# Kernel tuning notes

Hardware: AMD Instinct MI355X
Metric: run time of the kernel (lower is better)

The kernel has to match this reference:

```python
import jax, jax.numpy as jnp
import numpy as np


def setup_inputs() -> dict:
    key = jax.random.key(0)
    ks = jax.random.split(key, 7)
    B, C, H, W = 8, 1024, 64, 64
    heads, head_dim, red = 8, 128, 8
    s = 1.0 / np.sqrt(head_dim)
    return {
        "x": jax.random.normal(ks[0], (B, C, H, W), jnp.float32),
        "Wq": jax.random.normal(ks[1], (heads, red, head_dim), jnp.float32) * s,
        "bq": jax.random.normal(ks[2], (heads, red), jnp.float32) * s,
        "Wk": jax.random.normal(ks[3], (heads, red, head_dim), jnp.float32) * s,
        "bk": jax.random.normal(ks[4], (heads, red), jnp.float32) * s,
        "Wv": jax.random.normal(ks[5], (heads, head_dim, head_dim), jnp.float32) * s,
        "bv": jax.random.normal(ks[6], (heads, head_dim), jnp.float32) * s,
    }


def reference(x, Wq, bq, Wk, bk, Wv, bv):
    B, C, H, W = x.shape
    heads, red, d = Wq.shape  # d = head_dim
    # (B, heads, head_dim, HW)
    xh = x.reshape(B, heads, d, H * W)
    # per-head spatial average pool: (B, heads, head_dim)
    avg = jnp.mean(xh, axis=-1)
    # torch Linear: y = x @ W.T + b, applied per head
    q = jnp.einsum("bhds,hrd->bhsr", xh, Wq) + bq[None, :, None, :]   # (B,H,S,r)
    k = jnp.einsum("bhd,hrd->bhr", avg, Wk) + bk[None]                 # (B,H,r)
    v = jnp.einsum("bhd,hed->bhe", avg, Wv) + bv[None]                 # (B,H,d)
    # single-key attention; softmax over the spatial dim (torch dim=1)
    scores = jnp.einsum("bhsr,bhr->bhs", q, k)                          # (B,H,S)
    attn = jax.nn.softmax(scores, axis=-1)
    out = jnp.einsum("bhs,bhe->bhes", attn, v)                          # (B,H,d,S)
    return out.reshape(B, C, H, W)
```

## Files before the change

kernel.cpp:

```cpp
#include <hip/hip_runtime.h>
#include <math.h>

#define SDIM 4096
#define DDIM 128
#define RED 8
#define BATCH 8
#define BH 64
#define CH 1024

typedef float vfloat4 __attribute__((ext_vector_type(4)));

#define WS_V   8192
#define WS_SC  16384

__inline__ __device__ float wave_reduce_sum(float v) {
#pragma unroll
    for (int o = 32; o > 0; o >>= 1) v += __shfl_down(v, o, 64);
    return v;
}
__inline__ __device__ float wave_reduce_max(float v) {
#pragma unroll
    for (int o = 32; o > 0; o >>= 1) v = fmaxf(v, __shfl_down(v, o, 64));
    return v;
}

__global__ __launch_bounds__(256) void k_avg(const float* __restrict__ x,
                                             float* __restrict__ ws) {
    const int row = blockIdx.x;
    const int t = threadIdx.x;
    const float4* xr = (const float4*)(x + (size_t)row * SDIM);
    float s = 0.f;
#pragma unroll
    for (int p = 0; p < 4; ++p) {
        float4 v = xr[t + 256 * p];
        s += v.x + v.y + v.z + v.w;
    }
    s = wave_reduce_sum(s);
    __shared__ float part[4];
    const int wave = t >> 6, lane = t & 63;
    if (lane == 0) part[wave] = s;
    __syncthreads();
    if (t == 0) {
        float tot = part[0] + part[1] + part[2] + part[3];
        ws[row] = tot * (1.0f / SDIM);
    }
}

__global__ __launch_bounds__(256) void k_scores(
        const float* __restrict__ x,
        const float* __restrict__ Wq, const float* __restrict__ bq,
        const float* __restrict__ Wk, const float* __restrict__ bk,
        float* __restrict__ ws) {
    const int blk = blockIdx.x;
    const int bh = blk >> 3, chunk = blk & 7;
    const int b = bh >> 3, h = bh & 7;
    const int t = threadIdx.x;

    __shared__ float avgs[DDIM];
    __shared__ float kk[RED];
    __shared__ float wqs[DDIM];
    __shared__ float cc;

    if (t < DDIM) avgs[t] = ws[b * CH + h * DDIM + t];
    __syncthreads();
    if (t < RED) {
        const float* wkr = Wk + (h * RED + t) * DDIM;
        float acc = 0.f;
#pragma unroll 8
        for (int d = 0; d < DDIM; ++d) acc += wkr[d] * avgs[d];
        kk[t] = acc + bk[h * RED + t];
    }
    __syncthreads();
    if (t < DDIM) {
        float acc = 0.f;
#pragma unroll
        for (int r = 0; r < RED; ++r) acc += Wq[(h * RED + r) * DDIM + t] * kk[r];
        wqs[t] = acc;
    }
    if (t == 0) {
        float acc = 0.f;
#pragma unroll
        for (int r = 0; r < RED; ++r) acc += bq[h * RED + r] * kk[r];
        cc = acc;
    }
    __syncthreads();

    const int s0 = chunk * 512 + t * 2;
    const float* xb = x + (size_t)(b * CH + h * DDIM) * SDIM + s0;
    float2 acc;
    const float c = cc;
    acc.x = c; acc.y = c;
#pragma unroll 16
    for (int d = 0; d < DDIM; ++d) {
        float2 xv = *(const float2*)(xb + (size_t)d * SDIM);
        const float w = wqs[d];
        acc.x += xv.x * w; acc.y += xv.y * w;
    }
    *(float2*)(ws + WS_SC + (size_t)bh * SDIM + s0) = acc;
}

__global__ __launch_bounds__(256) void k_softmax_v(
        const float* __restrict__ Wv, const float* __restrict__ bv,
        float* __restrict__ ws) {
    const int bh = blockIdx.x;
    const int b = bh >> 3, h = bh & 7;
    const int t = threadIdx.x;

    __shared__ float avgs[DDIM];
    if (t < DDIM) avgs[t] = ws[b * CH + h * DDIM + t];
    __syncthreads();
    if (t < DDIM) {
        const float* wvr = Wv + (h * DDIM + t) * DDIM;
        float acc = 0.f;
#pragma unroll 8
        for (int d = 0; d < DDIM; ++d) acc += wvr[d] * avgs[d];
        ws[WS_V + bh * DDIM + t] = acc + bv[h * DDIM + t];
    }

    float4* sc = (float4*)(ws + WS_SC + (size_t)bh * SDIM);
    float4 vals[4];
    float m = -1e30f;
#pragma unroll
    for (int p = 0; p < 4; ++p) {
        vals[p] = sc[t + 256 * p];
        m = fmaxf(m, fmaxf(fmaxf(vals[p].x, vals[p].y), fmaxf(vals[p].z, vals[p].w)));
    }
    m = wave_reduce_max(m);
    __shared__ float smax[4];
    __shared__ float ssum[4];
    const int wave = t >> 6, lane = t & 63;
    if (lane == 0) smax[wave] = m;
    __syncthreads();
    const float gm = fmaxf(fmaxf(smax[0], smax[1]), fmaxf(smax[2], smax[3]));
    float sum = 0.f;
#pragma unroll
    for (int p = 0; p < 4; ++p) {
        vals[p].x = expf(vals[p].x - gm);
        vals[p].y = expf(vals[p].y - gm);
        vals[p].z = expf(vals[p].z - gm);
        vals[p].w = expf(vals[p].w - gm);
        sum += vals[p].x + vals[p].y + vals[p].z + vals[p].w;
    }
    sum = wave_reduce_sum(sum);
    if (lane == 0) ssum[wave] = sum;
    __syncthreads();
    const float inv = 1.0f / (ssum[0] + ssum[1] + ssum[2] + ssum[3]);
#pragma unroll
    for (int p = 0; p < 4; ++p) {
        float4 o;
        o.x = vals[p].x * inv; o.y = vals[p].y * inv;
        o.z = vals[p].z * inv; o.w = vals[p].w * inv;
        sc[t + 256 * p] = o;
    }
}

__global__ __launch_bounds__(256) void k_out(const float* __restrict__ ws,
                                             float* __restrict__ out) {
    const vfloat4* attn = (const vfloat4*)(ws + WS_SC);
    const float* vv = ws + WS_V;
    const size_t total = (size_t)BATCH * CH * (SDIM / 4);
    const size_t stride = (size_t)gridDim.x * blockDim.x;
    for (size_t f = (size_t)blockIdx.x * blockDim.x + threadIdx.x; f < total; f += stride) {
        const int s4 = (int)(f & 1023);
        const int ce = (int)((f >> 10) & 1023);
        const int b = (int)(f >> 20);
        const int bh = (b << 3) | (ce >> 7);
        const int e = ce & 127;
        const vfloat4 a = attn[bh * 1024 + s4];
        const float vx = vv[bh * 128 + e];
        vfloat4 o = a * vx;
        __builtin_nontemporal_store(o, ((vfloat4*)out) + f);
    }
}

extern "C" void kernel_launch(void* const* d_in, const int* in_sizes, int n_in,
                              void* d_out, int out_size, void* d_ws, size_t ws_size,
                              hipStream_t stream) {
    const float* x  = (const float*)d_in[0];
    const float* Wq = (const float*)d_in[1];
    const float* bq = (const float*)d_in[2];
    const float* bk = (const float*)d_in[4];
    const float* Wk = (const float*)d_in[3];
    const float* Wv = (const float*)d_in[5];
    const float* bv = (const float*)d_in[6];
    float* out = (float*)d_out;
    float* ws  = (float*)d_ws;

    k_avg<<<8192, 256, 0, stream>>>(x, ws);
    k_scores<<<512, 256, 0, stream>>>(x, Wq, bq, Wk, bk, ws);
    k_softmax_v<<<BH, 256, 0, stream>>>(Wv, bv, ws);
    k_out<<<8192, 256, 0, stream>>>(ws, out);
}
```

Baseline: 270.5 us.

## Fuse pipeline into single-pass cooperative kernel with per-rank query projections

```diff
diff --git a/kernel.cpp b/kernel.cpp
--- a/kernel.cpp
+++ b/kernel.cpp
@@ -1,5 +1,8 @@
 #include <hip/hip_runtime.h>
+#include <hip/hip_cooperative_groups.h>
 #include <math.h>
+
+namespace cg = cooperative_groups;
 
 #define SDIM 4096
 #define DDIM 128
@@ -10,8 +13,11 @@
 
 typedef float vfloat4 __attribute__((ext_vector_type(4)));
 
-#define WS_V   8192
-#define WS_SC  16384
+#define WS_SMAX 65536
+#define WS_SSUM 66048
+#define WS_VV   66560
+#define WS_ATT  74752
+#define WS_QR   336896
 
 __inline__ __device__ float wave_reduce_sum(float v) {
 #pragma unroll
@@ -24,111 +30,255 @@
     return v;
 }
 
-__global__ __launch_bounds__(256) void k_avg(const float* __restrict__ x,
-                                             float* __restrict__ ws) {
-    const int row = blockIdx.x;
-    const int t = threadIdx.x;
-    const float4* xr = (const float4*)(x + (size_t)row * SDIM);
-    float s = 0.f;
-#pragma unroll
-    for (int p = 0; p < 4; ++p) {
-        float4 v = xr[t + 256 * p];
-        s += v.x + v.y + v.z + v.w;
-    }
-    s = wave_reduce_sum(s);
-    __shared__ float part[4];
-    const int wave = t >> 6, lane = t & 63;
-    if (lane == 0) part[wave] = s;
-    __syncthreads();
-    if (t == 0) {
-        float tot = part[0] + part[1] + part[2] + part[3];
-        ws[row] = tot * (1.0f / SDIM);
-    }
-}
-
-__global__ __launch_bounds__(256) void k_scores(
+__global__ __launch_bounds__(256, 2) void k_fused(
         const float* __restrict__ x,
         const float* __restrict__ Wq, const float* __restrict__ bq,
         const float* __restrict__ Wk, const float* __restrict__ bk,
+        const float* __restrict__ Wv, const float* __restrict__ bv,
+        float* __restrict__ ws, float* __restrict__ out) {
+    const int blk = blockIdx.x;
+    const int bh = blk >> 3, chunk = blk & 7;
+    const int h = bh & 7;
+    const int t = threadIdx.x;
+    const int wave = t >> 6, lane = t & 63;
+
+    __shared__ float wqt[DDIM * RED];
+    __shared__ float avgp[DDIM * 4];
+    __shared__ float avgs[DDIM];
+    __shared__ float kk[RED];
+    __shared__ float bqs[RED];
+    __shared__ float vvs[DDIM];
+    __shared__ float attn[512];
+    __shared__ float red4[4];
+    __shared__ float gM, gInv;
+
+    for (int i = t; i < DDIM * RED; i += 256) {
+        const int d = i >> 3, r = i & 7;
+        wqt[i] = Wq[(h * RED + r) * DDIM + d];
+    }
+    __syncthreads();
+
+    const int s0 = chunk * 512 + t * 2;
+    const float* xb = x + (size_t)bh * DDIM * SDIM + s0;
+    float2 acc[RED];
+#pragma unroll
+    for (int r = 0; r < RED; ++r) acc[r] = make_float2(0.f, 0.f);
+
+#pragma unroll 8
+    for (int d = 0; d < DDIM; ++d) {
+        const float2 xv = *(const float2*)(xb + (size_t)d * SDIM);
+        const float4 wa = *(const float4*)&wqt[d * 8];
+        const float4 wb = *(const float4*)&wqt[d * 8 + 4];
+        acc[0].x += xv.x * wa.x; acc[0].y += xv.y * wa.x;
+        acc[1].x += xv.x * wa.y; acc[1].y += xv.y * wa.y;
+        acc[2].x += xv.x * wa.z; acc[2].y += xv.y * wa.z;
+        acc[3].x += xv.x * wa.w; acc[3].y += xv.y * wa.w;
+        acc[4].x += xv.x * wb.x; acc[4].y += xv.y * wb.x;
+        acc[5].x += xv.x * wb.y; acc[5].y += xv.y * wb.y;
+        acc[6].x += xv.x * wb.z; acc[6].y += xv.y * wb.z;
+        acc[7].x += xv.x * wb.w; acc[7].y += xv.y * wb.w;
+        float px = wave_reduce_sum(xv.x + xv.y);
+        if (lane == 0) avgp[d * 4 + wave] = px;
+    }
+    __syncthreads();
+    if (t < DDIM)
+        ws[chunk * 8192 + bh * DDIM + t] =
+            avgp[t * 4] + avgp[t * 4 + 1] + avgp[t * 4 + 2] + avgp[t * 4 + 3];
+
+    cg::this_grid().sync();
+
+    if (t < DDIM) {
+        float a = 0.f;
+#pragma unroll
+        for (int c = 0; c < 8; ++c) a += ws[c * 8192 + bh * DDIM + t];
+        avgs[t] = a * (1.0f / SDIM);
+    }
+    __syncthreads();
+    if (t < RED) {
+        const float* wkr = Wk + (h * RED + t) * DDIM;
+        float a = 0.f;
+#pragma unroll 8
+        for (int d = 0; d < DDIM; ++d) a += wkr[d] * avgs[d];
+        kk[t] = a + bk[h * RED + t];
+        bqs[t] = bq[h * RED + t];
+    }
+    if (t < DDIM) {
+        const float* wvr = Wv + (h * DDIM + t) * DDIM;
+        float a = 0.f;
+#pragma unroll 8
+        for (int d = 0; d < DDIM; ++d) a += wvr[d] * avgs[d];
+        vvs[t] = a + bv[h * DDIM + t];
+    }
+    __syncthreads();
+
+    float c0 = 0.f;
+#pragma unroll
+    for (int r = 0; r < RED; ++r) c0 += bqs[r] * kk[r];
+    float2 sc = make_float2(c0, c0);
+#pragma unroll
+    for (int r = 0; r < RED; ++r) {
+        sc.x += acc[r].x * kk[r];
+        sc.y += acc[r].y * kk[r];
+    }
+
+    float m = wave_reduce_max(fmaxf(sc.x, sc.y));
+    if (lane == 0) red4[wave] = m;
+    __syncthreads();
+    const float bm = fmaxf(fmaxf(red4[0], red4[1]), fmaxf(red4[2], red4[3]));
+    float ps = expf(sc.x - bm) + expf(sc.y - bm);
+    ps = wave_reduce_sum(ps);
+    __syncthreads();
+    if (lane == 0) red4[wave] = ps;
+    __syncthreads();
+    if (t == 0) {
+        ws[WS_SMAX + blk] = bm;
+        ws[WS_SSUM + blk] = red4[0] + red4[1] + red4[2] + red4[3];
+    }
+
+    cg::this_grid().sync();
+
+    if (t == 0) {
+        float pm[8];
+        float M = -1e30f;
+#pragma unroll
+        for (int c = 0; c < 8; ++c) {
+            pm[c] = ws[WS_SMAX + bh * 8 + c];
+            M = fmaxf(M, pm[c]);
+        }
+        float S = 0.f;
+#pragma unroll
+        for (int c = 0; c < 8; ++c) S += ws[WS_SSUM + bh * 8 + c] * expf(pm[c] - M);
+        gM = M;
+        gInv = 1.0f / S;
+    }
+    __syncthreads();
+    float2 a2;
+    a2.x = expf(sc.x - gM) * gInv;
+    a2.y = expf(sc.y - gM) * gInv;
+    *(float2*)&attn[t * 2] = a2;
+    __syncthreads();
+
+    const vfloat4 a4 = ((const vfloat4*)attn)[t & 127];
+    float* ob = out + (size_t)bh * DDIM * SDIM + chunk * 512;
+    const int ehalf = t >> 7;
+#pragma unroll 8
+    for (int i = 0; i < 64; ++i) {
+        const int e = i * 2 + ehalf;
+        vfloat4 o = a4 * vvs[e];
+        __builtin_nontemporal_store(o, (vfloat4*)(ob + (size_t)e * SDIM) + (t & 127));
+    }
+}
+
+__global__ __launch_bounds__(256, 2) void k_pass1(
+        const float* __restrict__ x, const float* __restrict__ Wq,
         float* __restrict__ ws) {
     const int blk = blockIdx.x;
     const int bh = blk >> 3, chunk = blk & 7;
-    const int b = bh >> 3, h = bh & 7;
+    const int h = bh & 7;
     const int t = threadIdx.x;
-
-    __shared__ float avgs[DDIM];
-    __shared__ float kk[RED];
-    __shared__ float wqs[DDIM];
+    const int wave = t >> 6, lane = t & 63;
+
+    __shared__ float wqt[DDIM * RED];
+    __shared__ float avgp[DDIM * 4];
+
+    for (int i = t; i < DDIM * RED; i += 256) {
+        const int d = i >> 3, r = i & 7;
+        wqt[i] = Wq[(h * RED + r) * DDIM + d];
+    }
+    __syncthreads();
+
+    const int s0 = chunk * 512 + t * 2;
+    const float* xb = x + (size_t)bh * DDIM * SDIM + s0;
+    float2 acc[RED];
+#pragma unroll
+    for (int r = 0; r < RED; ++r) acc[r] = make_float2(0.f, 0.f);
+
+#pragma unroll 8
+    for (int d = 0; d < DDIM; ++d) {
+        const float2 xv = *(const float2*)(xb + (size_t)d * SDIM);
+        const float4 wa = *(const float4*)&wqt[d * 8];
+        const float4 wb = *(const float4*)&wqt[d * 8 + 4];
+        acc[0].x += xv.x * wa.x; acc[0].y += xv.y * wa.x;
+        acc[1].x += xv.x * wa.y; acc[1].y += xv.y * wa.y;
+        acc[2].x += xv.x * wa.z; acc[2].y += xv.y * wa.z;
+        acc[3].x += xv.x * wa.w; acc[3].y += xv.y * wa.w;
+        acc[4].x += xv.x * wb.x; acc[4].y += xv.y * wb.x;
+        acc[5].x += xv.x * wb.y; acc[5].y += xv.y * wb.y;
+        acc[6].x += xv.x * wb.z; acc[6].y += xv.y * wb.z;
+        acc[7].x += xv.x * wb.w; acc[7].y += xv.y * wb.w;
+        float px = wave_reduce_sum(xv.x + xv.y);
+        if (lane == 0) avgp[d * 4 + wave] = px;
+    }
+#pragma unroll
+    for (int r = 0; r < RED; ++r)
+        *(float2*)(ws + WS_QR + ((size_t)(bh * RED + r)) * SDIM + s0) = acc[r];
+    __syncthreads();
+    if (t < DDIM)
+        ws[chunk * 8192 + bh * DDIM + t] =
+            avgp[t * 4] + avgp[t * 4 + 1] + avgp[t * 4 + 2] + avgp[t * 4 + 3];
+}
+
+__global__ __launch_bounds__(256) void k_mid(
+        const float* __restrict__ bq, const float* __restrict__ Wk,
+        const float* __restrict__ bk, const float* __restrict__ Wv,
+        const float* __restrict__ bv, float* __restrict__ ws) {
+    const int bh = blockIdx.x;
+    const int h = bh & 7;
+    const int t = threadIdx.x;
+    const int wave = t >> 6, lane = t & 63;
+
+    __shared__ float avgs[DDIM], kk[RED], bqs[RED];
+    __shared__ float smax[4], ssum[4];
     __shared__ float cc;
 
-    if (t < DDIM) avgs[t] = ws[b * CH + h * DDIM + t];
+    if (t < DDIM) {
+        float a = 0.f;
+#pragma unroll
+        for (int c = 0; c < 8; ++c) a += ws[c * 8192 + bh * DDIM + t];
+        avgs[t] = a * (1.0f / SDIM);
+    }
     __syncthreads();
     if (t < RED) {
         const float* wkr = Wk + (h * RED + t) * DDIM;
-        float acc = 0.f;
-#pragma unroll 8
-        for (int d = 0; d < DDIM; ++d) acc += wkr[d] * avgs[d];
-        kk[t] = acc + bk[h * RED + t];
-    }
-    __syncthreads();
-    if (t < DDIM) {
-        float acc = 0.f;
-#pragma unroll
-        for (int r = 0; r < RED; ++r) acc += Wq[(h * RED + r) * DDIM + t] * kk[r];
-        wqs[t] = acc;
-    }
-    if (t == 0) {
-        float acc = 0.f;
-#pragma unroll
-        for (int r = 0; r < RED; ++r) acc += bq[h * RED + r] * kk[r];
-        cc = acc;
-    }
-    __syncthreads();
-
-    const int s0 = chunk * 512 + t * 2;
-    const float* xb = x + (size_t)(b * CH + h * DDIM) * SDIM + s0;
-    float2 acc;
-    const float c = cc;
-    acc.x = c; acc.y = c;
-#pragma unroll 16
-    for (int d = 0; d < DDIM; ++d) {
-        float2 xv = *(const float2*)(xb + (size_t)d * SDIM);
-        const float w = wqs[d];
-        acc.x += xv.x * w; acc.y += xv.y * w;
-    }
-    *(float2*)(ws + WS_SC + (size_t)bh * SDIM + s0) = acc;
-}
-
-__global__ __launch_bounds__(256) void k_softmax_v(
-        const float* __restrict__ Wv, const float* __restrict__ bv,
-        float* __restrict__ ws) {
-    const int bh = blockIdx.x;
-    const int b = bh >> 3, h = bh & 7;
-    const int t = threadIdx.x;
-
-    __shared__ float avgs[DDIM];
-    if (t < DDIM) avgs[t] = ws[b * CH + h * DDIM + t];
-    __syncthreads();
+        float a = 0.f;
+#pragma unroll 8
+        for (int d = 0; d < DDIM; ++d) a += wkr[d] * avgs[d];
+        kk[t] = a + bk[h * RED + t];
+        bqs[t] = bq[h * RED + t];
+    }
     if (t < DDIM) {
         const float* wvr = Wv + (h * DDIM + t) * DDIM;
-        float acc = 0.f;
-#pragma unroll 8
-        for (int d = 0; d < DDIM; ++d) acc += wvr[d] * avgs[d];
-        ws[WS_V + bh * DDIM + t] = acc + bv[h * DDIM + t];
-    }
-
-    float4* sc = (float4*)(ws + WS_SC + (size_t)bh * SDIM);
+        float a = 0.f;
+#pragma unroll 8
+        for (int d = 0; d < DDIM; ++d) a += wvr[d] * avgs[d];
+        ws[WS_VV + bh * DDIM + t] = a + bv[h * DDIM + t];
+    }
+    __syncthreads();
+    if (t == 0) {
+        float a = 0.f;
+#pragma unroll
+        for (int r = 0; r < RED; ++r) a += bqs[r] * kk[r];
+        cc = a;
+    }
+    __syncthreads();
+
+    const float4* qr4 = (const float4*)(ws + WS_QR + (size_t)bh * RED * SDIM);
     float4 vals[4];
     float m = -1e30f;
 #pragma unroll
     for (int p = 0; p < 4; ++p) {
-        vals[p] = sc[t + 256 * p];
-        m = fmaxf(m, fmaxf(fmaxf(vals[p].x, vals[p].y), fmaxf(vals[p].z, vals[p].w)));
+        float4 a;
+        a.x = cc; a.y = cc; a.z = cc; a.w = cc;
+#pragma unroll
+        for (int r = 0; r < RED; ++r) {
+            const float4 q = qr4[r * 1024 + t + 256 * p];
+            const float kr = kk[r];
+            a.x += q.x * kr; a.y += q.y * kr; a.z += q.z * kr; a.w += q.w * kr;
+        }
+        vals[p] = a;
+        m = fmaxf(m, fmaxf(fmaxf(a.x, a.y), fmaxf(a.z, a.w)));
     }
     m = wave_reduce_max(m);
-    __shared__ float smax[4];
-    __shared__ float ssum[4];
-    const int wave = t >> 6, lane = t & 63;
     if (lane == 0) smax[wave] = m;
     __syncthreads();
     const float gm = fmaxf(fmaxf(smax[0], smax[1]), fmaxf(smax[2], smax[3]));
@@ -145,19 +295,20 @@
     if (lane == 0) ssum[wave] = sum;
     __syncthreads();
     const float inv = 1.0f / (ssum[0] + ssum[1] + ssum[2] + ssum[3]);
+    float4* att4 = (float4*)(ws + WS_ATT + (size_t)bh * SDIM);
 #pragma unroll
     for (int p = 0; p < 4; ++p) {
         float4 o;
         o.x = vals[p].x * inv; o.y = vals[p].y * inv;
         o.z = vals[p].z * inv; o.w = vals[p].w * inv;
-        sc[t + 256 * p] = o;
-    }
-}
-
-__global__ __launch_bounds__(256) void k_out(const float* __restrict__ ws,
-                                             float* __restrict__ out) {
-    const vfloat4* attn = (const vfloat4*)(ws + WS_SC);
-    const float* vv = ws + WS_V;
+        att4[t + 256 * p] = o;
+    }
+}
+
+__global__ __launch_bounds__(256) void k_bcast(const float* __restrict__ ws,
+                                               float* __restrict__ out) {
+    const vfloat4* attn = (const vfloat4*)(ws + WS_ATT);
+    const float* vv = ws + WS_VV;
     const size_t total = (size_t)BATCH * CH * (SDIM / 4);
     const size_t stride = (size_t)gridDim.x * blockDim.x;
     for (size_t f = (size_t)blockIdx.x * blockDim.x + threadIdx.x; f < total; f += stride) {
@@ -179,15 +330,20 @@
     const float* x  = (const float*)d_in[0];
     const float* Wq = (const float*)d_in[1];
     const float* bq = (const float*)d_in[2];
+    const float* Wk = (const float*)d_in[3];
     const float* bk = (const float*)d_in[4];
-    const float* Wk = (const float*)d_in[3];
     const float* Wv = (const float*)d_in[5];
     const float* bv = (const float*)d_in[6];
     float* out = (float*)d_out;
     float* ws  = (float*)d_ws;
 
-    k_avg<<<8192, 256, 0, stream>>>(x, ws);
-    k_scores<<<512, 256, 0, stream>>>(x, Wq, bq, Wk, bk, ws);
-    k_softmax_v<<<BH, 256, 0, stream>>>(Wv, bv, ws);
-    k_out<<<8192, 256, 0, stream>>>(ws, out);
-}
+    void* args[] = {(void*)&x, (void*)&Wq, (void*)&bq, (void*)&Wk, (void*)&bk,
+                    (void*)&Wv, (void*)&bv, (void*)&ws, (void*)&out};
+    hipError_t err = hipLaunchCooperativeKernel((const void*)k_fused, dim3(512),
+                                                dim3(256), args, 0, stream);
+    if (err != hipSuccess) {
+        k_pass1<<<512, 256, 0, stream>>>(x, Wq, ws);
+        k_mid<<<BH, 256, 0, stream>>>(bq, Wk, bk, Wv, bv, ws);
+        k_bcast<<<8192, 256, 0, stream>>>(ws, out);
+    }
+}
```

After: 428.1 us. +58.3%, slower.

## Fuse average pooling with per-rank query projection in one pass over x

Applied to the files above, without the earlier changes.

```diff
diff --git a/kernel.cpp b/kernel.cpp
--- a/kernel.cpp
+++ b/kernel.cpp
@@ -10,8 +10,11 @@
 
 typedef float vfloat4 __attribute__((ext_vector_type(4)));
 
-#define WS_V   8192
-#define WS_SC  16384
+#define WS_AVG  0
+#define WS_VV   32768
+#define WS_ATT  40960
+#define WS_QRP  303104
+#define QRP_DG  2097152
 
 __inline__ __device__ float wave_reduce_sum(float v) {
 #pragma unroll
@@ -24,111 +27,138 @@
     return v;
 }
 
-__global__ __launch_bounds__(256) void k_avg(const float* __restrict__ x,
-                                             float* __restrict__ ws) {
-    const int row = blockIdx.x;
-    const int t = threadIdx.x;
-    const float4* xr = (const float4*)(x + (size_t)row * SDIM);
-    float s = 0.f;
-#pragma unroll
-    for (int p = 0; p < 4; ++p) {
-        float4 v = xr[t + 256 * p];
-        s += v.x + v.y + v.z + v.w;
-    }
-    s = wave_reduce_sum(s);
-    __shared__ float part[4];
-    const int wave = t >> 6, lane = t & 63;
-    if (lane == 0) part[wave] = s;
-    __syncthreads();
-    if (t == 0) {
-        float tot = part[0] + part[1] + part[2] + part[3];
-        ws[row] = tot * (1.0f / SDIM);
-    }
-}
-
-__global__ __launch_bounds__(256) void k_scores(
-        const float* __restrict__ x,
-        const float* __restrict__ Wq, const float* __restrict__ bq,
-        const float* __restrict__ Wk, const float* __restrict__ bk,
+__global__ __launch_bounds__(256, 4) void k_qr(
+        const float* __restrict__ x, const float* __restrict__ Wq,
         float* __restrict__ ws) {
     const int blk = blockIdx.x;
-    const int bh = blk >> 3, chunk = blk & 7;
-    const int b = bh >> 3, h = bh & 7;
+    const int dg = blk & 3, chunk = (blk >> 2) & 3, bh = blk >> 4;
+    const int h = bh & 7;
     const int t = threadIdx.x;
-
-    __shared__ float avgs[DDIM];
-    __shared__ float kk[RED];
-    __shared__ float wqs[DDIM];
+    const int wave = t >> 6, lane = t & 63;
+    const int r8 = lane >> 3, seg = lane & 7;
+
+    __shared__ float wqt[32 * 8];
+    __shared__ float sxy[4][8][65];
+    __shared__ float fpart[4][4][8][9];
+
+    wqt[t] = Wq[(h * RED + (t & 7)) * DDIM + dg * 32 + (t >> 3)];
+    __syncthreads();
+
+    const int s0 = chunk * 1024 + t * 4;
+    const float* xb = x + (size_t)(bh * DDIM + dg * 32) * SDIM + s0;
+    vfloat4 accq[RED];
+#pragma unroll
+    for (int r = 0; r < RED; ++r) accq[r] = (vfloat4)0.f;
+
+#pragma unroll
+    for (int g = 0; g < 4; ++g) {
+#pragma unroll
+        for (int j = 0; j < 8; ++j) {
+            const int dl = g * 8 + j;
+            const vfloat4 xv = *(const vfloat4*)(xb + (size_t)dl * SDIM);
+            const float4 wa = *(const float4*)&wqt[dl * 8];
+            const float4 wb = *(const float4*)&wqt[dl * 8 + 4];
+            accq[0] += xv * wa.x;
+            accq[1] += xv * wa.y;
+            accq[2] += xv * wa.z;
+            accq[3] += xv * wa.w;
+            accq[4] += xv * wb.x;
+            accq[5] += xv * wb.y;
+            accq[6] += xv * wb.z;
+            accq[7] += xv * wb.w;
+            sxy[wave][j][lane] = xv[0] + xv[1] + xv[2] + xv[3];
+        }
+        float ps = 0.f;
+#pragma unroll
+        for (int j = 0; j < 8; ++j) ps += sxy[wave][r8][seg * 8 + j];
+        fpart[wave][g][r8][seg] = ps;
+    }
+
+    float* qb = ws + WS_QRP + (size_t)dg * QRP_DG + (size_t)(bh * RED) * SDIM + s0;
+#pragma unroll
+    for (int r = 0; r < RED; ++r)
+        *(vfloat4*)(qb + (size_t)r * SDIM) = accq[r];
+
+    __syncthreads();
+    if (t < 32) {
+        const int g = t >> 3, rr = t & 7;
+        float a = 0.f;
+#pragma unroll
+        for (int w = 0; w < 4; ++w)
+#pragma unroll
+            for (int s2 = 0; s2 < 8; ++s2)
+                a += fpart[w][g][rr][s2];
+        ws[WS_AVG + chunk * 8192 + bh * DDIM + dg * 32 + t] = a;
+    }
+}
+
+__global__ __launch_bounds__(256) void k_head(
+        const float* __restrict__ bq, const float* __restrict__ Wk,
+        const float* __restrict__ bk, const float* __restrict__ Wv,
+        const float* __restrict__ bv, float* __restrict__ ws) {
+    const int bh = blockIdx.x;
+    const int h = bh & 7;
+    const int t = threadIdx.x;
+    const int wave = t >> 6, lane = t & 63;
+
+    __shared__ float avgs[DDIM], kk[RED], bqs[RED];
+    __shared__ float smax[4], ssum[4];
     __shared__ float cc;
 
-    if (t < DDIM) avgs[t] = ws[b * CH + h * DDIM + t];
+    if (t < DDIM) {
+        float a = 0.f;
+#pragma unroll
+        for (int c = 0; c < 4; ++c) a += ws[WS_AVG + c * 8192 + bh * DDIM + t];
+        avgs[t] = a * (1.0f / SDIM);
+    }
     __syncthreads();
     if (t < RED) {
         const float* wkr = Wk + (h * RED + t) * DDIM;
-        float acc = 0.f;
+        float a = 0.f;
 #pragma unroll 8
-        for (int d = 0; d < DDIM; ++d) acc += wkr[d] * avgs[d];
-        kk[t] = acc + bk[h * RED + t];
-    }
-    __syncthreads();
-    if (t < DDIM) {
-        float acc = 0.f;
-#pragma unroll
-        for (int r = 0; r < RED; ++r) acc += Wq[(h * RED + r) * DDIM + t] * kk[r];
-        wqs[t] = acc;
-    }
-    if (t == 0) {
-        float acc = 0.f;
-#pragma unroll
-        for (int r = 0; r < RED; ++r) acc += bq[h * RED + r] * kk[r];
-        cc = acc;
-    }
-    __syncthreads();
-
-    const int s0 = chunk * 512 + t * 2;
-    const float* xb = x + (size_t)(b * CH + h * DDIM) * SDIM + s0;
-    float2 acc;
-    const float c = cc;
-    acc.x = c; acc.y = c;
-#pragma unroll 16
-    for (int d = 0; d < DDIM; ++d) {
-        float2 xv = *(const float2*)(xb + (size_t)d * SDIM);
-        const float w = wqs[d];
-        acc.x += xv.x * w; acc.y += xv.y * w;
-    }
-    *(float2*)(ws + WS_SC + (size_t)bh * SDIM + s0) = acc;
-}
-
-__global__ __launch_bounds__(256) void k_softmax_v(
-        const float* __restrict__ Wv, const float* __restrict__ bv,
-        float* __restrict__ ws) {
-    const int bh = blockIdx.x;
-    const int b = bh >> 3, h = bh & 7;
-    const int t = threadIdx.x;
-
-    __shared__ float avgs[DDIM];
-    if (t < DDIM) avgs[t] = ws[b * CH + h * DDIM + t];
-    __syncthreads();
+        for (int d = 0; d < DDIM; ++d) a += wkr[d] * avgs[d];
+        kk[t] = a + bk[h * RED + t];
+        bqs[t] = bq[h * RED + t];
+    }
     if (t < DDIM) {
         const float* wvr = Wv + (h * DDIM + t) * DDIM;
-        float acc = 0.f;
+        float a = 0.f;
 #pragma unroll 8
-        for (int d = 0; d < DDIM; ++d) acc += wvr[d] * avgs[d];
-        ws[WS_V + bh * DDIM + t] = acc + bv[h * DDIM + t];
-    }
-
-    float4* sc = (float4*)(ws + WS_SC + (size_t)bh * SDIM);
+        for (int d = 0; d < DDIM; ++d) a += wvr[d] * avgs[d];
+        ws[WS_VV + bh * DDIM + t] = a + bv[h * DDIM + t];
+    }
+    __syncthreads();
+    if (t == 0) {
+        float a = 0.f;
+#pragma unroll
+        for (int r = 0; r < RED; ++r) a += bqs[r] * kk[r];
+        cc = a;
+    }
+    __syncthreads();
+
     float4 vals[4];
     float m = -1e30f;
 #pragma unroll
     for (int p = 0; p < 4; ++p) {
-        vals[p] = sc[t + 256 * p];
-        m = fmaxf(m, fmaxf(fmaxf(vals[p].x, vals[p].y), fmaxf(vals[p].z, vals[p].w)));
+        float4 a;
+        a.x = cc; a.y = cc; a.z = cc; a.w = cc;
+#pragma unroll
+        for (int r = 0; r < RED; ++r) {
+            const size_t base = WS_QRP + (size_t)(bh * RED + r) * SDIM + (t + 256 * p) * 4;
+            float4 q0 = *(const float4*)(ws + base);
+            float4 q1 = *(const float4*)(ws + base + QRP_DG);
+            float4 q2 = *(const float4*)(ws + base + 2 * (size_t)QRP_DG);
+            float4 q3 = *(const float4*)(ws + base + 3 * (size_t)QRP_DG);
+            const float kr = kk[r];
+            a.x += (q0.x + q1.x + q2.x + q3.x) * kr;
+            a.y += (q0.y + q1.y + q2.y + q3.y) * kr;
+            a.z += (q0.z + q1.z + q2.z + q3.z) * kr;
+            a.w += (q0.w + q1.w + q2.w + q3.w) * kr;
+        }
+        vals[p] = a;
+        m = fmaxf(m, fmaxf(fmaxf(a.x, a.y), fmaxf(a.z, a.w)));
     }
     m = wave_reduce_max(m);
-    __shared__ float smax[4];
-    __shared__ float ssum[4];
-    const int wave = t >> 6, lane = t & 63;
     if (lane == 0) smax[wave] = m;
     __syncthreads();
     const float gm = fmaxf(fmaxf(smax[0], smax[1]), fmaxf(smax[2], smax[3]));
@@ -145,31 +175,36 @@
     if (lane == 0) ssum[wave] = sum;
     __syncthreads();
     const float inv = 1.0f / (ssum[0] + ssum[1] + ssum[2] + ssum[3]);
+    float4* att4 = (float4*)(ws + WS_ATT + (size_t)bh * SDIM);
 #pragma unroll
     for (int p = 0; p < 4; ++p) {
         float4 o;
         o.x = vals[p].x * inv; o.y = vals[p].y * inv;
         o.z = vals[p].z * inv; o.w = vals[p].w * inv;
-        sc[t + 256 * p] = o;
-    }
-}
-
-__global__ __launch_bounds__(256) void k_out(const float* __restrict__ ws,
-                                             float* __restrict__ out) {
-    const vfloat4* attn = (const vfloat4*)(ws + WS_SC);
-    const float* vv = ws + WS_V;
-    const size_t total = (size_t)BATCH * CH * (SDIM / 4);
-    const size_t stride = (size_t)gridDim.x * blockDim.x;
-    for (size_t f = (size_t)blockIdx.x * blockDim.x + threadIdx.x; f < total; f += stride) {
-        const int s4 = (int)(f & 1023);
-        const int ce = (int)((f >> 10) & 1023);
-        const int b = (int)(f >> 20);
-        const int bh = (b << 3) | (ce >> 7);
-        const int e = ce & 127;
-        const vfloat4 a = attn[bh * 1024 + s4];
-        const float vx = vv[bh * 128 + e];
-        vfloat4 o = a * vx;
-        __builtin_nontemporal_store(o, ((vfloat4*)out) + f);
+        att4[t + 256 * p] = o;
+    }
+}
+
+__global__ __launch_bounds__(256) void k_wr(const float* __restrict__ ws,
+                                            float* __restrict__ out) {
+    const int blk = blockIdx.x;
+    const int bh = blk >> 4, chunk = blk & 15;
+    const int t = threadIdx.x;
+    const int wave = t >> 6, lane = t & 63;
+
+    __shared__ float vvs[DDIM];
+    if (t < DDIM) vvs[t] = ws[WS_VV + bh * DDIM + t];
+
+    const vfloat4 a4 =
+        ((const vfloat4*)(ws + WS_ATT))[bh * 1024 + chunk * 64 + lane];
+    __syncthreads();
+
+    vfloat4* ob = (vfloat4*)out + (size_t)(bh * DDIM) * 1024 + chunk * 64 + lane;
+#pragma unroll
+    for (int i = 0; i < 32; ++i) {
+        const int e = wave * 32 + i;
+        vfloat4 o = a4 * vvs[e];
+        __builtin_nontemporal_store(o, ob + (size_t)e * 1024);
     }
 }
 
@@ -179,15 +214,14 @@
     const float* x  = (const float*)d_in[0];
     const float* Wq = (const float*)d_in[1];
     const float* bq = (const float*)d_in[2];
+    const float* Wk = (const float*)d_in[3];
     const float* bk = (const float*)d_in[4];
-    const float* Wk = (const float*)d_in[3];
     const float* Wv = (const float*)d_in[5];
     const float* bv = (const float*)d_in[6];
     float* out = (float*)d_out;
     float* ws  = (float*)d_ws;
 
-    k_avg<<<8192, 256, 0, stream>>>(x, ws);
-    k_scores<<<512, 256, 0, stream>>>(x, Wq, bq, Wk, bk, ws);
-    k_softmax_v<<<BH, 256, 0, stream>>>(Wv, bv, ws);
-    k_out<<<8192, 256, 0, stream>>>(ws, out);
-}
+    k_qr<<<1024, 256, 0, stream>>>(x, Wq, ws);
+    k_head<<<BH, 256, 0, stream>>>(bq, Wk, bk, Wv, bv, ws);
+    k_wr<<<1024, 256, 0, stream>>>(ws, out);
+}
```

Result: slower. 276.3 us (+2.1%).
